# Performance work log

Hardware: AMD Instinct MI355X
Metric: run time of the kernel (lower is better)

## Reference

```python
import jax, jax.numpy as jnp
import numpy as np


def setup_inputs() -> dict:
    key = jax.random.key(0)
    k1, k2, k3 = jax.random.split(key, 3)
    B, D, C = 16384, 1024, 14
    z_image = jax.random.normal(k1, (B, D), dtype=jnp.float32)
    z_text = jax.random.normal(k2, (B, D), dtype=jnp.float32)
    labels = jax.random.randint(k3, (B, C), 0, 2, dtype=jnp.int32)
    return {"z_image": z_image, "z_text": z_text, "labels": labels}


def _margins(labels):
    # labels: [B, C] binary; imposter index j = (i+1) % B -> roll by -1
    lj = jnp.roll(labels, -1, axis=0)
    equal = jnp.all(labels == lj, axis=1)                     # [B]
    n = jnp.sum(labels | lj, axis=1).astype(jnp.float32)      # union size
    d = jnp.sum(labels ^ lj, axis=1).astype(jnp.float32)      # hamming diff
    m = jnp.where(n > 0, jnp.maximum(0.5, d / jnp.maximum(n, 1.0)), 0.5)
    return jnp.where(equal, 0.0, m)                           # [B]


def reference(z_image, z_text, labels):
    # similarity_function == 'dot' (default path of the torch module)
    margin = _margins(labels)                                  # [B]
    paired = jnp.sum(z_image * z_text, axis=1)                 # dot(img_i, txt_i)
    imp_img = jnp.sum(jnp.roll(z_image, -1, axis=0) * z_text, axis=1)  # dot(img_j, txt_i)
    imp_txt = jnp.sum(jnp.roll(z_text, -1, axis=0) * z_image, axis=1)  # dot(txt_j, img_i)
    loss_img = jnp.mean(jax.nn.relu(imp_img - paired + margin))
    loss_txt = jnp.mean(jax.nn.relu(imp_txt - paired + margin))
    return loss_img + loss_txt
```

## Files before the change

kernel.cpp:

```cpp
#include <hip/hip_runtime.h>


constexpr int D   = 1024;
constexpr int C   = 14;
constexpr int RPB = 4;
constexpr int WPB = 4;

__device__ __forceinline__ float dot4(const float4 x, const float4 y) {
    return x.x * y.x + x.y * y.y + x.z * y.z + x.w * y.w;
}

__global__ __launch_bounds__(256) void rank_phase1(
    const float* __restrict__ zi, const float* __restrict__ zt,
    const int* __restrict__ labels, float* __restrict__ partial, int B)
{
    const int wave = threadIdx.x >> 6;
    const int lane = threadIdx.x & 63;

    const int nwg = gridDim.x;
    const int wg  = (blockIdx.x & 7) * (nwg >> 3) + (blockIdx.x >> 3);

    const int r0 = wg * RPB;
    const int M  = B - 1;

    const int idx = (wave << 6) + lane;

    int lx = 0, lo = 0;
    {
        const int kk = lane >> 4, c = lane & 15;
        if (wave == 0 && c < C) {
            const int ra = (r0 + kk)     & M;
            const int rb = (r0 + kk + 1) & M;
            const int li = labels[(size_t)ra * C + c];
            const int lj = labels[(size_t)rb * C + c];
            lx = li ^ lj;
            lo = li | lj;
        }
    }

    float4 a[RPB + 1], b[RPB + 1];
    #pragma unroll
    for (int k = 0; k <= RPB; ++k) {
        const int r = (r0 + k) & M;
        a[k] = ((const float4*)(zi + (size_t)r * D))[idx];
        b[k] = ((const float4*)(zt + (size_t)r * D))[idx];
    }

    float v[12];
    #pragma unroll
    for (int k = 0; k < RPB; ++k) {
        v[k]     = dot4(a[k],     b[k]);
        v[4 + k] = dot4(a[k + 1], b[k]);
        v[8 + k] = dot4(b[k + 1], a[k]);
    }

    #pragma unroll
    for (int off = 32; off > 0; off >>= 1) {
        #pragma unroll
        for (int i = 0; i < 12; ++i) v[i] += __shfl_down(v[i], off, 64);
    }

    __shared__ float red[WPB][12];
    if (lane == 0) {
        #pragma unroll
        for (int i = 0; i < 12; ++i) red[wave][i] = v[i];
    }
    __syncthreads();

    if (wave == 0) {
        const unsigned long long bx = __ballot(lx != 0);
        const unsigned long long bo = __ballot(lo != 0);
        if (lane == 0) {
            float local = 0.f;
            #pragma unroll
            for (int k = 0; k < RPB; ++k) {
                const float p  = red[0][k]     + red[1][k]     + red[2][k]     + red[3][k];
                const float di = red[0][4 + k] + red[1][4 + k] + red[2][4 + k] + red[3][4 + k];
                const float dt = red[0][8 + k] + red[1][8 + k] + red[2][8 + k] + red[3][8 + k];
                const float dv = (float)__popcll((bx >> (16 * k)) & 0x3FFFull);
                const float nv = (float)__popcll((bo >> (16 * k)) & 0x3FFFull);
                const float m  = (dv == 0.f) ? 0.f : fmaxf(0.5f, dv / nv);
                local += fmaxf(di - p + m, 0.f) + fmaxf(dt - p + m, 0.f);
            }
            partial[wg] = local;
        }
    }
}

__global__ __launch_bounds__(256) void rank_phase2(
    const float* __restrict__ partial, float* __restrict__ out,
    int npart, float invB)
{
    float s = 0.f;
    for (int i = threadIdx.x; i < npart; i += 256) s += partial[i];
    #pragma unroll
    for (int off = 32; off > 0; off >>= 1) s += __shfl_down(s, off, 64);
    __shared__ float sm[4];
    if ((threadIdx.x & 63) == 0) sm[threadIdx.x >> 6] = s;
    __syncthreads();
    if (threadIdx.x == 0)
        out[0] = (sm[0] + sm[1] + sm[2] + sm[3]) * invB;
}

extern "C" void kernel_launch(void* const* d_in, const int* in_sizes, int n_in,
                              void* d_out, int out_size, void* d_ws, size_t ws_size,
                              hipStream_t stream) {
    const float* zi     = (const float*)d_in[0];
    const float* zt     = (const float*)d_in[1];
    const int*   labels = (const int*)d_in[2];
    float*       out    = (float*)d_out;
    float*       ws     = (float*)d_ws;

    const int B      = in_sizes[0] / D;
    const int blocks = B / RPB;

    rank_phase1<<<blocks, 256, 0, stream>>>(zi, zt, labels, ws, B);
    rank_phase2<<<1, 256, 0, stream>>>(ws, out, blocks, 1.0f / (float)B);
}
```

Measured before the change: 161.6 us.

## Process 16 rows per block with chunked prefetch and parallel margin computation

```diff
diff --git a/kernel.cpp b/kernel.cpp
--- a/kernel.cpp
+++ b/kernel.cpp
@@ -3,7 +3,7 @@
 
 constexpr int D   = 1024;
 constexpr int C   = 14;
-constexpr int RPB = 4;
+constexpr int RPB = 16;
 constexpr int WPB = 4;
 
 __device__ __forceinline__ float dot4(const float4 x, const float4 y) {
@@ -20,70 +20,93 @@
     const int nwg = gridDim.x;
     const int wg  = (blockIdx.x & 7) * (nwg >> 3) + (blockIdx.x >> 3);
 
-    const int r0 = wg * RPB;
-    const int M  = B - 1;
-
+    const int r0  = wg * RPB;
+    const int M   = B - 1;
     const int idx = (wave << 6) + lane;
 
-    int lx = 0, lo = 0;
+    __shared__ float red[WPB][48];
+    __shared__ float mlds[RPB];
+
     {
         const int kk = lane >> 4, c = lane & 15;
-        if (wave == 0 && c < C) {
-            const int ra = (r0 + kk)     & M;
-            const int rb = (r0 + kk + 1) & M;
+        int lx = 0, lo = 0;
+        if (c < C) {
+            const int ra = (r0 + 4 * wave + kk) & M;
+            const int rb = (ra + 1) & M;
             const int li = labels[(size_t)ra * C + c];
             const int lj = labels[(size_t)rb * C + c];
             lx = li ^ lj;
             lo = li | lj;
         }
+        const unsigned long long bx = __ballot(lx != 0);
+        const unsigned long long bo = __ballot(lo != 0);
+        if (lane < 4) {
+            const float dv = (float)__popcll((bx >> (16 * lane)) & 0x3FFFull);
+            const float nv = (float)__popcll((bo >> (16 * lane)) & 0x3FFFull);
+            mlds[4 * wave + lane] = (dv == 0.f) ? 0.f : fmaxf(0.5f, dv / nv);
+        }
     }
 
-    float4 a[RPB + 1], b[RPB + 1];
+    float v[48];
     #pragma unroll
-    for (int k = 0; k <= RPB; ++k) {
+    for (int i = 0; i < 48; ++i) v[i] = 0.f;
+
+    float4 a[5], b[5], na[4], nb[4];
+    #pragma unroll
+    for (int k = 0; k < 5; ++k) {
         const int r = (r0 + k) & M;
         a[k] = ((const float4*)(zi + (size_t)r * D))[idx];
         b[k] = ((const float4*)(zt + (size_t)r * D))[idx];
     }
 
-    float v[12];
     #pragma unroll
-    for (int k = 0; k < RPB; ++k) {
-        v[k]     = dot4(a[k],     b[k]);
-        v[4 + k] = dot4(a[k + 1], b[k]);
-        v[8 + k] = dot4(b[k + 1], a[k]);
+    for (int cch = 0; cch < 4; ++cch) {
+        if (cch < 3) {
+            #pragma unroll
+            for (int j = 0; j < 4; ++j) {
+                const int r = (r0 + 4 * cch + 5 + j) & M;
+                na[j] = ((const float4*)(zi + (size_t)r * D))[idx];
+                nb[j] = ((const float4*)(zt + (size_t)r * D))[idx];
+            }
+        }
+        #pragma unroll
+        for (int k = 0; k < 4; ++k) {
+            v[4 * cch + k]      += dot4(a[k],     b[k]);
+            v[16 + 4 * cch + k] += dot4(a[k + 1], b[k]);
+            v[32 + 4 * cch + k] += dot4(b[k + 1], a[k]);
+        }
+        if (cch < 3) {
+            a[0] = a[4]; b[0] = b[4];
+            #pragma unroll
+            for (int j = 0; j < 4; ++j) { a[j + 1] = na[j]; b[j + 1] = nb[j]; }
+        }
     }
 
     #pragma unroll
     for (int off = 32; off > 0; off >>= 1) {
         #pragma unroll
-        for (int i = 0; i < 12; ++i) v[i] += __shfl_down(v[i], off, 64);
+        for (int i = 0; i < 48; ++i) v[i] += __shfl_down(v[i], off, 64);
     }
-
-    __shared__ float red[WPB][12];
     if (lane == 0) {
         #pragma unroll
-        for (int i = 0; i < 12; ++i) red[wave][i] = v[i];
+        for (int i = 0; i < 48; ++i) red[wave][i] = v[i];
     }
     __syncthreads();
 
-    if (wave == 0) {
-        const unsigned long long bx = __ballot(lx != 0);
-        const unsigned long long bo = __ballot(lo != 0);
-        if (lane == 0) {
-            float local = 0.f;
-            #pragma unroll
-            for (int k = 0; k < RPB; ++k) {
-                const float p  = red[0][k]     + red[1][k]     + red[2][k]     + red[3][k];
-                const float di = red[0][4 + k] + red[1][4 + k] + red[2][4 + k] + red[3][4 + k];
-                const float dt = red[0][8 + k] + red[1][8 + k] + red[2][8 + k] + red[3][8 + k];
-                const float dv = (float)__popcll((bx >> (16 * k)) & 0x3FFFull);
-                const float nv = (float)__popcll((bo >> (16 * k)) & 0x3FFFull);
-                const float m  = (dv == 0.f) ? 0.f : fmaxf(0.5f, dv / nv);
-                local += fmaxf(di - p + m, 0.f) + fmaxf(dt - p + m, 0.f);
-            }
-            partial[wg] = local;
+    if (wave == 0 && lane < RPB) {
+        float P = 0.f, I = 0.f, T = 0.f;
+        #pragma unroll
+        for (int w = 0; w < WPB; ++w) {
+            P += red[w][lane];
+            I += red[w][16 + lane];
+            T += red[w][32 + lane];
         }
+        const float m = mlds[lane];
+        float local = fmaxf(I - P + m, 0.f) + fmaxf(T - P + m, 0.f);
+        #pragma unroll
+        for (int off = 8; off > 0; off >>= 1)
+            local += __shfl_down(local, off, 16);
+        if (lane == 0) partial[wg] = local;
     }
 }
 
```

After: 158.6 us. No clear change (-1.9%).
